# Kernel optimization log

Hardware: AMD Instinct MI355X
Metric: run time of the kernel (lower is better)

Reference implementation:

```python
import jax, jax.numpy as jnp
import numpy as np

KG_E = 50000
KG_R = 500
E_DIM = 300
NE = 400000      # entity-entity adjacency nnz
NEER = 400000    # entity-entity-relation triples
ALPHA1 = 0.1
ALPHA2 = 0.3
LRELU_ALPHA = 0.2


def setup_inputs() -> dict:
    key = jax.random.key(0)
    ks = jax.random.split(key, 13)
    primal_e_0 = jax.random.normal(ks[0], (KG_E, E_DIM), jnp.float32)
    # sparse-ish relation->entity incidence matrices (dense storage as in torch code)
    r_head = (jax.random.uniform(ks[1], (KG_R, KG_E)) < 0.01).astype(jnp.float32)
    r_tail = (jax.random.uniform(ks[2], (KG_R, KG_E)) < 0.01).astype(jnp.float32)
    e_adj_index = jax.random.randint(ks[3], (2, NE), 0, KG_E)
    e_adj_data = jax.random.uniform(ks[4], (NE,), jnp.float32)
    eer_adj_index = jax.random.randint(ks[5], (2, NEER), 0, KG_E)
    eer_adj_data = jax.random.randint(ks[6], (NEER,), 0, KG_R)
    s = 0.05
    be_L = jax.random.normal(ks[7], (KG_E, 1), jnp.float32) * s
    be_R = jax.random.normal(ks[8], (KG_E, 1), jnp.float32) * s
    atten_r = jax.random.normal(ks[9], (2 * E_DIM, 1), jnp.float32) * s
    gcnW1 = jax.random.normal(ks[10], (E_DIM, E_DIM), jnp.float32) * s
    highwayWr = jax.random.normal(ks[11], (E_DIM, E_DIM), jnp.float32) * s
    highwaybr = jax.random.normal(ks[12], (E_DIM, 1), jnp.float32) * s
    return {"primal_e_0": primal_e_0, "r_head": r_head, "r_tail": r_tail,
            "e_adj_data": e_adj_data, "be_L": be_L, "be_R": be_R,
            "atten_r": atten_r, "gcnW1": gcnW1, "highwayWr": highwayWr,
            "highwaybr": highwaybr, "e_adj_index": e_adj_index,
            "eer_adj_index": eer_adj_index, "eer_adj_data": eer_adj_data}


def _spmm(idx, data, x):
    # sparse [KG_E, KG_E] (COO rows=idx[0], cols=idx[1], vals=data) @ dense x
    rows, cols = idx[0], idx[1]
    return jax.ops.segment_sum(data[:, None] * x[cols], rows, num_segments=KG_E)


def _inv_or_zero(x):
    return jnp.where(x == 0, 0.0, 1.0 / x)


def _add_r_layer(e, be_L, be_R, r_head, r_tail, rh_inv, rt_inv):
    L_r = (r_head @ (e * be_L)) * rh_inv   # [KG_R, E_DIM]
    R_r = (r_tail @ (e * be_R)) * rt_inv
    return jax.nn.relu(jnp.concatenate([L_r, R_r], axis=-1))  # [KG_R, 2*E_DIM]


def _add_e_att_layer(e, r_layer, eer_idx, eer_rel, atten_r):
    rows, cols = eer_idx[0], eer_idx[1]
    e_ij = jnp.concatenate([e[rows], e[cols]], axis=1)           # [NEER, 2*E_DIM]
    eer_embed = e_ij * r_layer[eer_rel]                           # [NEER, 2*E_DIM]
    score = (eer_embed @ atten_r)[:, 0]                           # [NEER]
    ee_atten = jnp.exp(-jax.nn.leaky_relu(score, LRELU_ALPHA))
    e_rowsum = jax.ops.segment_sum(ee_atten, rows, num_segments=KG_E)[:, None]
    e_rowsum = _inv_or_zero(e_rowsum)
    e_out = jax.ops.segment_sum(ee_atten[:, None] * e[cols], rows, num_segments=KG_E)
    return jax.nn.relu(e_out * e_rowsum)


def _add_diag_layer(e, gcnW1, e_adj_index, e_adj_data):
    # dropout p=0 (eval) -> identity
    return jax.nn.relu(_spmm(e_adj_index, e_adj_data, e @ gcnW1))


def _highway(e1, e2, Wr, br):
    gate = jax.nn.sigmoid(e1 @ Wr + br[:, 0])
    return gate * e2 + (1.0 - gate) * e1


def reference(primal_e_0, r_head, r_tail, e_adj_data, be_L, be_R, atten_r,
              gcnW1, highwayWr, highwaybr, e_adj_index, eer_adj_index,
              eer_adj_data):
    rh_inv = _inv_or_zero(jnp.sum(r_head, axis=-1, keepdims=True))
    rt_inv = _inv_or_zero(jnp.sum(r_tail, axis=-1, keepdims=True))
    name_embed = primal_e_0
    r1 = _add_r_layer(name_embed, be_L, be_R, r_head, r_tail, rh_inv, rt_inv)
    e1 = _add_e_att_layer(name_embed, r1, eer_adj_index, eer_adj_data, atten_r)
    e1 = name_embed + ALPHA1 * e1
    r2 = _add_r_layer(e1, be_L, be_R, r_head, r_tail, rh_inv, rt_inv)
    e2 = _add_e_att_layer(e1, r2, eer_adj_index, eer_adj_data, atten_r)
    e2 = name_embed + ALPHA2 * e2
    g1 = _add_diag_layer(e2, gcnW1, e_adj_index, e_adj_data)
    g2 = _highway(e2, g1, highwayWr, highwaybr)
    g3 = _add_diag_layer(g2, gcnW1, e_adj_index, e_adj_data)
    return _highway(g2, g3, highwayWr, highwaybr)
```

## Files before the change

### kernel.cpp

```cpp
#include <hip/hip_runtime.h>
#include <math.h>

#define KG_E  50000
#define KG_R  500
#define E_DIM 300
#define NPAIR 150
#define NP2   75
#define CAP   1024
#define LRELU 0.2f

#define NK    10
#define NT    40
#define XS_LD 328

#define NB_SCAN 49

typedef __attribute__((ext_vector_type(8))) short bf16x8;
typedef __attribute__((ext_vector_type(4))) float f32x4;

__device__ __forceinline__ unsigned short f2bf(float x) {
  union { float f; unsigned u; } v; v.f = x;
  unsigned r = v.u + 0x7FFFu + ((v.u >> 16) & 1u);
  return (unsigned short)(r >> 16);
}
__device__ __forceinline__ float bf2f(unsigned short x) {
  union { unsigned u; float f; } v; v.u = ((unsigned)x) << 16; return v.f;
}
__device__ __forceinline__ float plo(unsigned u) {
  union { unsigned u; float f; } v; v.u = u << 16; return v.f;
}
__device__ __forceinline__ float phi(unsigned u) {
  union { unsigned u; float f; } v; v.u = u & 0xFFFF0000u; return v.f;
}
__device__ __forceinline__ unsigned packbf(float lo, float hi) {
  return (unsigned)f2bf(lo) | ((unsigned)f2bf(hi) << 16);
}

__global__ __launch_bounds__(256) void k_tobf(
    const float* __restrict__ src, unsigned short* __restrict__ dst, int n4)
{
  int i = blockIdx.x * 256 + threadIdx.x;
  if (i >= n4) return;
  float4 f = ((const float4*)src)[i];
  ushort4 o;
  o.x = f2bf(f.x); o.y = f2bf(f.y); o.z = f2bf(f.z); o.w = f2bf(f.w);
  ((ushort4*)dst)[i] = o;
}

#define NCH 5
#define SCAP 1024
__global__ __launch_bounds__(256) void k_compact2(
    const float* __restrict__ r_head, const float* __restrict__ r_tail,
    const float* __restrict__ be_L, const float* __restrict__ be_R,
    int* __restrict__ lidx, float* __restrict__ lsval,
    int* __restrict__ fill, float* __restrict__ rsum)
{
  __shared__ int   ls_e[SCAP];
  __shared__ float ls_v[SCAP];
  __shared__ int   ls_cnt;
  __shared__ float ls_sum;
  __shared__ int   ls_base;
  int m = blockIdx.z;
  int r = blockIdx.y;
  const float* rowp = (m ? r_tail : r_head) + (size_t)r * KG_E;
  const float* be   = m ? be_R : be_L;
  int slot = m * KG_R + r;
  int lane = threadIdx.x & 63;
  if (threadIdx.x == 0) { ls_cnt = 0; ls_sum = 0.f; }
  __syncthreads();

  const int CH = KG_E / NCH;
  int c0 = blockIdx.x * CH;
  const float4* rp4 = (const float4*)(rowp + c0);
  float lsum = 0.f;
  for (int i = threadIdx.x; i < CH / 4; i += 256) {
    float4 f = rp4[i];
    float vs[4] = {f.x, f.y, f.z, f.w};
    #pragma unroll
    for (int q = 0; q < 4; ++q) {
      float v = vs[q];
      lsum += v;
      bool nz = (v != 0.f);
      unsigned long long mask = __ballot(nz);
      if (mask) {
        int leader = (int)__ffsll(mask) - 1;
        int wbase = 0;
        if (lane == leader) wbase = atomicAdd(&ls_cnt, (int)__popcll(mask));
        wbase = __shfl(wbase, leader, 64);
        if (nz) {
          int pos = wbase + (int)__popcll(mask & ((1ULL << lane) - 1));
          if (pos < SCAP) {
            int e = c0 + 4 * i + q;
            ls_e[pos] = e;
            ls_v[pos] = v * be[e];
          }
        }
      }
    }
  }
  #pragma unroll
  for (int off = 32; off > 0; off >>= 1) lsum += __shfl_xor(lsum, off, 64);
  if (lane == 0 && lsum != 0.f) atomicAdd(&ls_sum, lsum);
  __syncthreads();

  int total = ls_cnt < SCAP ? ls_cnt : SCAP;
  if (threadIdx.x == 0) {
    ls_base = atomicAdd(&fill[slot], total);
    if (ls_sum != 0.f) atomicAdd(&rsum[slot], ls_sum);
  }
  __syncthreads();
  int gbase = ls_base;
  int*   li = lidx  + (size_t)slot * CAP;
  float* lv = lsval + (size_t)slot * CAP;
  for (int i = threadIdx.x; i < total; i += 256) {
    int pos = gbase + i;
    if (pos < CAP) { li[pos] = ls_e[i]; lv[pos] = ls_v[i]; }
  }
}

__global__ __launch_bounds__(256) void k_rmeta(
    const int* __restrict__ fill, const float* __restrict__ rsum,
    int* __restrict__ cnt, float* __restrict__ inv)
{
  int i = blockIdx.x * 256 + threadIdx.x;
  if (i < 2 * KG_R) {
    int c = fill[i];
    cnt[i] = c > CAP ? CAP : c;
    float s = rsum[i];
    inv[i] = (s == 0.f) ? 0.f : 1.f / s;
  }
}

__global__ __launch_bounds__(192) void k_rlayer(
    const unsigned short* __restrict__ Eb, const int* __restrict__ lidx,
    const float* __restrict__ lsval, const int* __restrict__ cnt,
    const float* __restrict__ inv, const float* __restrict__ atten,
    unsigned* __restrict__ wpk)
{
  int b = blockIdx.x;
  int m = b / KG_R, r = b % KG_R;
  int p = threadIdx.x;
  if (p >= NPAIR) return;
  int slot = m * KG_R + r;
  int n = cnt[slot];
  const int*   li = lidx  + (size_t)slot * CAP;
  const float* lv = lsval + (size_t)slot * CAP;
  float alo = 0.f, ahi = 0.f;
  #pragma unroll 4
  for (int i = 0; i < n; ++i) {
    int e = li[i];
    float s = lv[i];
    unsigned u = ((const unsigned*)(Eb + (size_t)e * E_DIM))[p];
    alo += s * plo(u);
    ahi += s * phi(u);
  }
  float iv = inv[slot];
  float vlo = alo * iv; vlo = vlo > 0.f ? vlo : 0.f;
  float vhi = ahi * iv; vhi = vhi > 0.f ? vhi : 0.f;
  vlo *= atten[m * E_DIM + 2 * p];
  vhi *= atten[m * E_DIM + 2 * p + 1];
  wpk[(size_t)slot * NPAIR + p] = packbf(vlo, vhi);
}

__global__ __launch_bounds__(256) void k_hist(
    const int* __restrict__ rows, int* __restrict__ cnt, int n)
{
  int i = blockIdx.x * 256 + threadIdx.x;
  if (i < n) atomicAdd(&cnt[rows[i]], 1);
}

__global__ __launch_bounds__(256) void k_scan_a(
    const int* __restrict__ c0, const int* __restrict__ c1,
    int* __restrict__ bsum, int n)
{
  const int* c = blockIdx.y ? c1 : c0;
  int base = blockIdx.x * 1024;
  int s = 0;
  #pragma unroll
  for (int k = 0; k < 4; ++k) {
    int i = base + k * 256 + threadIdx.x;
    if (i < n) s += c[i];
  }
  #pragma unroll
  for (int off = 32; off > 0; off >>= 1) s += __shfl_xor(s, off, 64);
  __shared__ int ws[4];
  if ((threadIdx.x & 63) == 0) ws[threadIdx.x >> 6] = s;
  __syncthreads();
  if (threadIdx.x == 0)
    bsum[blockIdx.y * (NB_SCAN + 1) + blockIdx.x] = ws[0] + ws[1] + ws[2] + ws[3];
}

__global__ __launch_bounds__(64) void k_scan_b(int* __restrict__ bsum)
{
  if (threadIdx.x < 2) {
    int* b = bsum + threadIdx.x * (NB_SCAN + 1);
    int acc = 0;
    for (int i = 0; i < NB_SCAN; ++i) { int v = b[i]; b[i] = acc; acc += v; }
    b[NB_SCAN] = acc;
  }
}

__global__ __launch_bounds__(256) void k_scan_c(
    const int* __restrict__ c0, const int* __restrict__ c1,
    const int* __restrict__ bsum,
    int* __restrict__ s0, int* __restrict__ s1, int n)
{
  const int* c = blockIdx.y ? c1 : c0;
  int* sO = blockIdx.y ? s1 : s0;
  if (blockIdx.x == 0 && threadIdx.x == 0)
    sO[n] = bsum[blockIdx.y * (NB_SCAN + 1) + NB_SCAN];
  int boff = bsum[blockIdx.y * (NB_SCAN + 1) + blockIdx.x];
  int i0 = blockIdx.x * 1024 + threadIdx.x * 4;
  int4 v = {0, 0, 0, 0};
  if (i0 < n) v = ((const int4*)c)[i0 >> 2];
  int tsum = v.x + v.y + v.z + v.w;
  int lane = threadIdx.x & 63, wid = threadIdx.x >> 6;
  int inc = tsum;
  #pragma unroll
  for (int off = 1; off < 64; off <<= 1) {
    int u = __shfl_up(inc, off, 64);
    if (lane >= off) inc += u;
  }
  __shared__ int ws[4];
  if (lane == 63) ws[wid] = inc;
  __syncthreads();
  int woff = 0;
  if (wid > 0) woff += ws[0];
  if (wid > 1) woff += ws[1];
  if (wid > 2) woff += ws[2];
  int ex = boff + woff + inc - tsum;
  if (i0 < n) {
    int4 o;
    o.x = ex; o.y = ex + v.x; o.z = o.y + v.y; o.w = o.z + v.z;
    ((int4*)sO)[i0 >> 2] = o;
  }
}

__global__ __launch_bounds__(256) void k_scatter_eer(
    const int* __restrict__ eidx, const int* __restrict__ erel,
    const int* __restrict__ start, int* __restrict__ fill,
    int* __restrict__ scol, int* __restrict__ srel, int neer)
{
  int i = blockIdx.x * 256 + threadIdx.x;
  if (i >= neer) return;
  int row = eidx[i];
  int pos = start[row] + atomicAdd(&fill[row], 1);
  scol[pos] = eidx[neer + i];
  srel[pos] = erel[i];
}

__global__ __launch_bounds__(256) void k_scatter_adj(
    const int* __restrict__ aidx, const float* __restrict__ adata,
    const int* __restrict__ start, int* __restrict__ fill,
    int* __restrict__ scol, float* __restrict__ sval, int ne)
{
  int i = blockIdx.x * 256 + threadIdx.x;
  if (i >= ne) return;
  int row = aidx[i];
  int pos = start[row] + atomicAdd(&fill[row], 1);
  scol[pos] = aidx[ne + i];
  sval[pos] = adata[i];
}

__global__ __launch_bounds__(256) void k_att_csr(
    const unsigned short* __restrict__ Eb, const unsigned* __restrict__ wpk,
    const int* __restrict__ start, const int* __restrict__ scol,
    const int* __restrict__ srel, const unsigned short* __restrict__ baseb,
    float alpha, unsigned short* __restrict__ outb)
{
  int wave = threadIdx.x >> 6, lane = threadIdx.x & 63;
  int half = lane >> 5, hl = lane & 31;
  int row = blockIdx.x * 4 + wave;
  if (row >= KG_E) return;
  int s = start[row], e = start[row + 1];
  const uint2* erp = (const uint2*)(Eb + (size_t)row * E_DIM);
  float er0[3], er1[3], er2[3], er3[3];
  float ac0[3] = {0,0,0}, ac1[3] = {0,0,0}, ac2[3] = {0,0,0}, ac3[3] = {0,0,0};
  #pragma unroll
  for (int c = 0; c < 3; ++c) {
    int m = c * 32 + hl;
    if (m < NP2) {
      uint2 u = erp[m];
      er0[c] = plo(u.x); er1[c] = phi(u.x); er2[c] = plo(u.y); er3[c] = phi(u.y);
    } else { er0[c] = er1[c] = er2[c] = er3[c] = 0.f; }
  }
  float rs = 0.f;
  int nIter = (e - s + 1) >> 1;
  for (int it = 0; it < nIter; ++it) {
    int j = s + 2 * it + half;
    bool act = j < e;
    int col = act ? scol[j] : 0;
    int rel = act ? srel[j] : 0;
    const uint2* ecp = (const uint2*)(Eb + (size_t)col * E_DIM);
    const uint2* whp = (const uint2*)(wpk + (size_t)rel * NPAIR);
    const uint2* wtp = (const uint2*)(wpk + (size_t)(KG_R + rel) * NPAIR);
    float e0[3], e1[3], e2[3], e3[3];
    float p4 = 0.f;
    #pragma unroll
    for (int c = 0; c < 3; ++c) {
      int m = c * 32 + hl;
      if (m < NP2) {
        uint2 uc = ecp[m], uh = whp[m], ut = wtp[m];
        float c0 = plo(uc.x), c1 = phi(uc.x), c2 = plo(uc.y), c3 = phi(uc.y);
        e0[c] = c0; e1[c] = c1; e2[c] = c2; e3[c] = c3;
        p4 += er0[c] * plo(uh.x) + er1[c] * phi(uh.x)
            + er2[c] * plo(uh.y) + er3[c] * phi(uh.y)
            + c0 * plo(ut.x) + c1 * phi(ut.x)
            + c2 * plo(ut.y) + c3 * phi(ut.y);
      } else { e0[c] = e1[c] = e2[c] = e3[c] = 0.f; }
    }
    #pragma unroll
    for (int off = 16; off > 0; off >>= 1) p4 += __shfl_xor(p4, off, 64);
    float la = p4 >= 0.f ? p4 : LRELU * p4;
    float at = act ? __expf(-la) : 0.f;
    rs += at;
    #pragma unroll
    for (int c = 0; c < 3; ++c) {
      ac0[c] += at * e0[c]; ac1[c] += at * e1[c];
      ac2[c] += at * e2[c]; ac3[c] += at * e3[c];
    }
  }
  rs += __shfl_xor(rs, 32, 64);
  #pragma unroll
  for (int c = 0; c < 3; ++c) {
    ac0[c] += __shfl_xor(ac0[c], 32, 64);
    ac1[c] += __shfl_xor(ac1[c], 32, 64);
    ac2[c] += __shfl_xor(ac2[c], 32, 64);
    ac3[c] += __shfl_xor(ac3[c], 32, 64);
  }
  if (half == 0) {
    float iv = (rs == 0.f) ? 0.f : 1.f / rs;
    const uint2* bp = (const uint2*)(baseb + (size_t)row * E_DIM);
    uint2* op = (uint2*)(outb + (size_t)row * E_DIM);
    #pragma unroll
    for (int c = 0; c < 3; ++c) {
      int m = c * 32 + hl;
      if (m < NP2) {
        uint2 ub = bp[m];
        float v0 = ac0[c] * iv; v0 = v0 > 0.f ? v0 : 0.f;
        float v1 = ac1[c] * iv; v1 = v1 > 0.f ? v1 : 0.f;
        float v2 = ac2[c] * iv; v2 = v2 > 0.f ? v2 : 0.f;
        float v3 = ac3[c] * iv; v3 = v3 > 0.f ? v3 : 0.f;
        uint2 o2;
        o2.x = packbf(plo(ub.x) + alpha * v0, phi(ub.x) + alpha * v1);
        o2.y = packbf(plo(ub.y) + alpha * v2, phi(ub.y) + alpha * v3);
        op[m] = o2;
      }
    }
  }
}

__global__ __launch_bounds__(256) void k_spmm_hw(
    const unsigned short* __restrict__ Xb, const int* __restrict__ start,
    const int* __restrict__ scol, const float* __restrict__ sval,
    const unsigned short* __restrict__ Gb, const unsigned short* __restrict__ baseb,
    const float* __restrict__ br,
    unsigned short* __restrict__ outb, float* __restrict__ outf)
{
  int wave = threadIdx.x >> 6, lane = threadIdx.x & 63;
  int half = lane >> 5, hl = lane & 31;
  int row = blockIdx.x * 4 + wave;
  if (row >= KG_E) return;
  int s = start[row], e = start[row + 1];
  float ac0[3] = {0,0,0}, ac1[3] = {0,0,0}, ac2[3] = {0,0,0}, ac3[3] = {0,0,0};
  int nIter = (e - s + 1) >> 1;
  for (int it = 0; it < nIter; ++it) {
    int j = s + 2 * it + half;
    bool act = j < e;
    int col = act ? scol[j] : 0;
    float v = act ? sval[j] : 0.f;
    const uint2* xp = (const uint2*)(Xb + (size_t)col * E_DIM);
    #pragma unroll
    for (int c = 0; c < 3; ++c) {
      int m = c * 32 + hl;
      if (m < NP2) {
        uint2 u = xp[m];
        ac0[c] += v * plo(u.x); ac1[c] += v * phi(u.x);
        ac2[c] += v * plo(u.y); ac3[c] += v * phi(u.y);
      }
    }
  }
  #pragma unroll
  for (int c = 0; c < 3; ++c) {
    ac0[c] += __shfl_xor(ac0[c], 32, 64);
    ac1[c] += __shfl_xor(ac1[c], 32, 64);
    ac2[c] += __shfl_xor(ac2[c], 32, 64);
    ac3[c] += __shfl_xor(ac3[c], 32, 64);
  }
  if (half == 0) {
    const uint2* gp = (const uint2*)(Gb + (size_t)row * E_DIM);
    const uint2* bp = (const uint2*)(baseb + (size_t)row * E_DIM);
    #pragma unroll
    for (int c = 0; c < 3; ++c) {
      int m = c * 32 + hl;
      if (m < NP2) {
        uint2 ug = gp[m], ub = bp[m];
        float4 b4 = ((const float4*)br)[m];
        float g0 = 1.f / (1.f + __expf(-(plo(ug.x) + b4.x)));
        float g1 = 1.f / (1.f + __expf(-(phi(ug.x) + b4.y)));
        float g2 = 1.f / (1.f + __expf(-(plo(ug.y) + b4.z)));
        float g3 = 1.f / (1.f + __expf(-(phi(ug.y) + b4.w)));
        float y0 = ac0[c] > 0.f ? ac0[c] : 0.f;
        float y1 = ac1[c] > 0.f ? ac1[c] : 0.f;
        float y2 = ac2[c] > 0.f ? ac2[c] : 0.f;
        float y3 = ac3[c] > 0.f ? ac3[c] : 0.f;
        float o0 = g0 * y0 + (1.f - g0) * plo(ub.x);
        float o1 = g1 * y1 + (1.f - g1) * phi(ub.x);
        float o2 = g2 * y2 + (1.f - g2) * plo(ub.y);
        float o3 = g3 * y3 + (1.f - g3) * phi(ub.y);
        if (outb) {
          uint2 ov;
          ov.x = packbf(o0, o1); ov.y = packbf(o2, o3);
          ((uint2*)(outb + (size_t)row * E_DIM))[m] = ov;
        } else {
          float4 of; of.x = o0; of.y = o1; of.z = o2; of.w = o3;
          ((float4*)(outf + (size_t)row * E_DIM))[m] = of;
        }
      }
    }
  }
}

__global__ __launch_bounds__(64) void k_packW(
    const float* __restrict__ W1, const float* __restrict__ W2,
    unsigned short* __restrict__ Wp)
{
  int lane = threadIdx.x;
  int t = blockIdx.x, s = blockIdx.y;
  int c = t * 16 + (lane & 15);
  unsigned short v[8];
  #pragma unroll
  for (int j = 0; j < 8; ++j) {
    int k = s * 32 + (lane >> 4) * 8 + j;
    float x = 0.f;
    if (k < E_DIM && c < 2 * E_DIM)
      x = (c < E_DIM) ? W1[(size_t)k * E_DIM + c]
                      : W2[(size_t)k * E_DIM + (c - E_DIM)];
    v[j] = f2bf(x);
  }
  size_t base = ((size_t)(t * NK + s) * 64 + lane) * 8;
  #pragma unroll
  for (int j = 0; j < 8; ++j) Wp[base + j] = v[j];
}

__global__ __launch_bounds__(256) void k_gemm2_mfma(
    const unsigned short* __restrict__ Xb, const unsigned short* __restrict__ Wp,
    unsigned short* __restrict__ Y1, unsigned short* __restrict__ Y2, int M)
{
  __shared__ unsigned short Xs[32][XS_LD];
  int tid = threadIdx.x;
  int r0 = blockIdx.x * 32;
  int nb = blockIdx.y;

  for (int t = tid; t < 32 * (XS_LD / 2); t += 256) {
    int r = t / (XS_LD / 2), u = t % (XS_LD / 2);
    unsigned v = 0;
    int rg = r0 + r;
    if (rg < M && u < E_DIM / 2) v = ((const unsigned*)Xb)[(size_t)rg * (E_DIM / 2) + u];
    ((unsigned*)&Xs[0][0])[r * (XS_LD / 2) + u] = v;
  }
  __syncthreads();

  int wid = tid >> 6, lane = tid & 63;
  int wave_m = wid >> 1, wave_n = wid & 1;
  int rowA = wave_m * 16 + (lane & 15);
  int kgrp = (lane >> 4) * 8;
  int tb0 = nb * 8 + wave_n * 4;

  const bf16x8* wfrag = (const bf16x8*)Wp + (size_t)tb0 * (NK * 64) + lane;

  f32x4 acc[4] = {{0,0,0,0},{0,0,0,0},{0,0,0,0},{0,0,0,0}};
  #pragma unroll 2
  for (int ks = 0; ks < NK; ++ks) {
    bf16x8 a = *(const bf16x8*)&Xs[rowA][ks * 32 + kgrp];
    #pragma unroll
    for (int nt = 0; nt < 4; ++nt) {
      bf16x8 b = wfrag[(nt * NK + ks) * 64];
      acc[nt] = __builtin_amdgcn_mfma_f32_16x16x32_bf16(a, b, acc[nt], 0, 0, 0);
    }
  }

  int rbase = r0 + wave_m * 16 + ((lane >> 4) << 2);
  #pragma unroll
  for (int nt = 0; nt < 4; ++nt) {
    int c = (tb0 + nt) * 16 + (lane & 15);
    #pragma unroll
    for (int j = 0; j < 4; ++j) {
      int row = rbase + j;
      if (row < M) {
        unsigned short hv = f2bf(acc[nt][j]);
        if (c < E_DIM)            Y1[(size_t)row * E_DIM + c] = hv;
        else if (c < 2 * E_DIM)   Y2[(size_t)row * E_DIM + (c - E_DIM)] = hv;
      }
    }
  }
}

extern "C" void kernel_launch(void* const* d_in, const int* in_sizes, int n_in,
                              void* d_out, int out_size, void* d_ws, size_t ws_size,
                              hipStream_t stream)
{
  const float* primal      = (const float*)d_in[0];
  const float* r_head      = (const float*)d_in[1];
  const float* r_tail      = (const float*)d_in[2];
  const float* e_adj_data  = (const float*)d_in[3];
  const float* be_L        = (const float*)d_in[4];
  const float* be_R        = (const float*)d_in[5];
  const float* atten_r     = (const float*)d_in[6];
  const float* gcnW1       = (const float*)d_in[7];
  const float* hwWr        = (const float*)d_in[8];
  const float* hwbr        = (const float*)d_in[9];
  const int*   e_adj_index = (const int*)d_in[10];
  const int*   eer_idx     = (const int*)d_in[11];
  const int*   eer_rel     = (const int*)d_in[12];
  int ne   = in_sizes[10] / 2;
  int neer = in_sizes[11] / 2;

  char* ws = (char*)d_ws;
  size_t off = 0;
  auto take = [&](size_t bytes) {
    void* p = ws + off;
    off = (off + bytes + 255) & ~(size_t)255;
    return p;
  };
  int*   cnt      = (int*)  take((size_t)2 * KG_R * sizeof(int));
  float* inv      = (float*)take((size_t)2 * KG_R * sizeof(float));
  size_t z0 = off;
  int*   hcntA    = (int*)  take((size_t)KG_E * sizeof(int));
  int*   hcntB    = (int*)  take((size_t)KG_E * sizeof(int));
  int*   hfillA   = (int*)  take((size_t)KG_E * sizeof(int));
  int*   hfillB   = (int*)  take((size_t)KG_E * sizeof(int));
  int*   rfill    = (int*)  take((size_t)2 * KG_R * sizeof(int));
  float* rsumb    = (float*)take((size_t)2 * KG_R * sizeof(float));
  size_t z1 = off;
  int*   lidx     = (int*)  take((size_t)2 * KG_R * CAP * sizeof(int));
  float* lsv      = (float*)take((size_t)2 * KG_R * CAP * sizeof(float));
  unsigned* wpk   = (unsigned*)take((size_t)2 * KG_R * NPAIR * sizeof(unsigned));
  int*   bsum     = (int*)  take((size_t)2 * (NB_SCAN + 1) * sizeof(int));
  int*   eer_start= (int*)  take((size_t)(KG_E + 4) * sizeof(int));
  int*   adj_start= (int*)  take((size_t)(KG_E + 4) * sizeof(int));
  int*   eer_scol = (int*)  take((size_t)neer * sizeof(int));
  int*   eer_srel = (int*)  take((size_t)neer * sizeof(int));
  int*   adj_scol = (int*)  take((size_t)ne * sizeof(int));
  float* adj_sval = (float*)take((size_t)ne * sizeof(float));
  unsigned short* Wp = (unsigned short*)take((size_t)NT * NK * 64 * 8 * sizeof(unsigned short));
  unsigned short* B0 = (unsigned short*)take((size_t)KG_E * E_DIM * sizeof(unsigned short));
  unsigned short* B1 = (unsigned short*)take((size_t)KG_E * E_DIM * sizeof(unsigned short));
  unsigned short* B2 = (unsigned short*)take((size_t)KG_E * E_DIM * sizeof(unsigned short));
  unsigned short* Fb = (unsigned short*)take((size_t)KG_E * E_DIM * sizeof(unsigned short));
  unsigned short* Gb = (unsigned short*)take((size_t)KG_E * E_DIM * sizeof(unsigned short));
  float* out      = (float*)d_out;
  (void)ws_size; (void)n_in; (void)out_size;

  int eg = (neer + 255) / 256;
  int ag = (ne + 255) / 256;

  hipMemsetAsync(ws + z0, 0, z1 - z0, stream);

  k_hist<<<eg, 256, 0, stream>>>(eer_idx, hcntA, neer);
  k_hist<<<ag, 256, 0, stream>>>(e_adj_index, hcntB, ne);
  k_scan_a<<<dim3(NB_SCAN, 2), 256, 0, stream>>>(hcntA, hcntB, bsum, KG_E);
  k_scan_b<<<1, 64, 0, stream>>>(bsum);
  k_scan_c<<<dim3(NB_SCAN, 2), 256, 0, stream>>>(hcntA, hcntB, bsum,
                                                 eer_start, adj_start, KG_E);
  k_scatter_eer<<<eg, 256, 0, stream>>>(eer_idx, eer_rel, eer_start, hfillA,
                                        eer_scol, eer_srel, neer);
  k_scatter_adj<<<ag, 256, 0, stream>>>(e_adj_index, e_adj_data, adj_start, hfillB,
                                        adj_scol, adj_sval, ne);

  k_compact2<<<dim3(NCH, KG_R, 2), 256, 0, stream>>>(r_head, r_tail, be_L, be_R,
                                                     lidx, lsv, rfill, rsumb);
  k_rmeta<<<(2 * KG_R + 255) / 256, 256, 0, stream>>>(rfill, rsumb, cnt, inv);
  k_packW<<<dim3(NT, NK), 64, 0, stream>>>(gcnW1, hwWr, Wp);
  int n4 = KG_E * E_DIM / 4;
  k_tobf<<<(n4 + 255) / 256, 256, 0, stream>>>(primal, B0, n4);

  int rg = (KG_E + 3) / 4;

  k_rlayer<<<2 * KG_R, 192, 0, stream>>>(B0, lidx, lsv, cnt, inv, atten_r, wpk);
  k_att_csr<<<rg, 256, 0, stream>>>(B0, wpk, eer_start, eer_scol, eer_srel,
                                    B0, 0.1f, B1);
  k_rlayer<<<2 * KG_R, 192, 0, stream>>>(B1, lidx, lsv, cnt, inv, atten_r, wpk);
  k_att_csr<<<rg, 256, 0, stream>>>(B1, wpk, eer_start, eer_scol, eer_srel,
                                    B0, 0.3f, B2);

  dim3 gg((KG_E + 31) / 32, 5);
  k_gemm2_mfma<<<gg, 256, 0, stream>>>(B2, Wp, Fb, Gb, KG_E);
  k_spmm_hw<<<rg, 256, 0, stream>>>(Fb, adj_start, adj_scol, adj_sval,
                                    Gb, B2, hwbr, B1, (float*)nullptr);

  k_gemm2_mfma<<<gg, 256, 0, stream>>>(B1, Wp, Fb, Gb, KG_E);
  k_spmm_hw<<<rg, 256, 0, stream>>>(Fb, adj_start, adj_scol, adj_sval,
                                    Gb, B1, hwbr, (unsigned short*)nullptr, out);
}
```

Measured before the change: 830.9 us.

## Switch intermediate storage and attention math from bf16 to fp16 packed ops

Changes every bf16 intermediate buffer, the packed weights and the MFMA GEMM to fp16, and does the attention kernel's dot products and weighted accumulation with packed half2 FMAs instead of scalar fp32. The aim is to cut per-edge ALU work in the gather-heavy attention kernel and to use cheaper packed conversions. It adds risk of precision loss or overflow, since attention accumulators now sum in fp16, and fp16 has a narrower range than bf16.

```diff
diff --git a/kernel.cpp b/kernel.cpp
--- a/kernel.cpp
+++ b/kernel.cpp
@@ -1,4 +1,5 @@
 #include <hip/hip_runtime.h>
+#include <hip/hip_fp16.h>
 #include <math.h>
 
 #define KG_E  50000
@@ -15,36 +16,31 @@
 
 #define NB_SCAN 49
 
-typedef __attribute__((ext_vector_type(8))) short bf16x8;
+typedef __attribute__((ext_vector_type(8))) _Float16 f16x8;
 typedef __attribute__((ext_vector_type(4))) float f32x4;
 
-__device__ __forceinline__ unsigned short f2bf(float x) {
-  union { float f; unsigned u; } v; v.f = x;
-  unsigned r = v.u + 0x7FFFu + ((v.u >> 16) & 1u);
-  return (unsigned short)(r >> 16);
-}
-__device__ __forceinline__ float bf2f(unsigned short x) {
-  union { unsigned u; float f; } v; v.u = ((unsigned)x) << 16; return v.f;
-}
-__device__ __forceinline__ float plo(unsigned u) {
-  union { unsigned u; float f; } v; v.u = u << 16; return v.f;
-}
-__device__ __forceinline__ float phi(unsigned u) {
-  union { unsigned u; float f; } v; v.u = u & 0xFFFF0000u; return v.f;
-}
-__device__ __forceinline__ unsigned packbf(float lo, float hi) {
-  return (unsigned)f2bf(lo) | ((unsigned)f2bf(hi) << 16);
-}
-
-__global__ __launch_bounds__(256) void k_tobf(
-    const float* __restrict__ src, unsigned short* __restrict__ dst, int n4)
+__device__ __forceinline__ __half2 u2h2(unsigned u) {
+  union { unsigned u; __half2 h; } v; v.u = u; return v.h;
+}
+__device__ __forceinline__ unsigned h22u(__half2 h) {
+  union { unsigned u; __half2 h; } v; v.h = h; return v.u;
+}
+__device__ __forceinline__ float hlo(unsigned u) { return __low2float(u2h2(u)); }
+__device__ __forceinline__ float hhi(unsigned u) { return __high2float(u2h2(u)); }
+__device__ __forceinline__ unsigned packh(float lo, float hi) {
+  return h22u(__floats2half2_rn(lo, hi));
+}
+
+__global__ __launch_bounds__(256) void k_toh(
+    const float* __restrict__ src, __half* __restrict__ dst, int n4)
 {
   int i = blockIdx.x * 256 + threadIdx.x;
   if (i >= n4) return;
   float4 f = ((const float4*)src)[i];
-  ushort4 o;
-  o.x = f2bf(f.x); o.y = f2bf(f.y); o.z = f2bf(f.z); o.w = f2bf(f.w);
-  ((ushort4*)dst)[i] = o;
+  uint2 o;
+  o.x = packh(f.x, f.y);
+  o.y = packh(f.z, f.w);
+  ((uint2*)dst)[i] = o;
 }
 
 #define NCH 5
@@ -132,7 +128,7 @@
 }
 
 __global__ __launch_bounds__(192) void k_rlayer(
-    const unsigned short* __restrict__ Eb, const int* __restrict__ lidx,
+    const __half* __restrict__ Eb, const int* __restrict__ lidx,
     const float* __restrict__ lsval, const int* __restrict__ cnt,
     const float* __restrict__ inv, const float* __restrict__ atten,
     unsigned* __restrict__ wpk)
@@ -151,15 +147,15 @@
     int e = li[i];
     float s = lv[i];
     unsigned u = ((const unsigned*)(Eb + (size_t)e * E_DIM))[p];
-    alo += s * plo(u);
-    ahi += s * phi(u);
+    alo += s * hlo(u);
+    ahi += s * hhi(u);
   }
   float iv = inv[slot];
   float vlo = alo * iv; vlo = vlo > 0.f ? vlo : 0.f;
   float vhi = ahi * iv; vhi = vhi > 0.f ? vhi : 0.f;
   vlo *= atten[m * E_DIM + 2 * p];
   vhi *= atten[m * E_DIM + 2 * p + 1];
-  wpk[(size_t)slot * NPAIR + p] = packbf(vlo, vhi);
+  wpk[(size_t)slot * NPAIR + p] = packh(vlo, vhi);
 }
 
 __global__ __launch_bounds__(256) void k_hist(
@@ -263,10 +259,10 @@
 }
 
 __global__ __launch_bounds__(256) void k_att_csr(
-    const unsigned short* __restrict__ Eb, const unsigned* __restrict__ wpk,
+    const __half* __restrict__ Eb, const unsigned* __restrict__ wpk,
     const int* __restrict__ start, const int* __restrict__ scol,
-    const int* __restrict__ srel, const unsigned short* __restrict__ baseb,
-    float alpha, unsigned short* __restrict__ outb)
+    const int* __restrict__ srel, const __half* __restrict__ baseb,
+    float alpha, __half* __restrict__ outb)
 {
   int wave = threadIdx.x >> 6, lane = threadIdx.x & 63;
   int half = lane >> 5, hl = lane & 31;
@@ -274,15 +270,16 @@
   if (row >= KG_E) return;
   int s = start[row], e = start[row + 1];
   const uint2* erp = (const uint2*)(Eb + (size_t)row * E_DIM);
-  float er0[3], er1[3], er2[3], er3[3];
-  float ac0[3] = {0,0,0}, ac1[3] = {0,0,0}, ac2[3] = {0,0,0}, ac3[3] = {0,0,0};
+  __half2 zero2 = __floats2half2_rn(0.f, 0.f);
+  __half2 er[3][2], ac[3][2];
   #pragma unroll
   for (int c = 0; c < 3; ++c) {
     int m = c * 32 + hl;
     if (m < NP2) {
       uint2 u = erp[m];
-      er0[c] = plo(u.x); er1[c] = phi(u.x); er2[c] = plo(u.y); er3[c] = phi(u.y);
-    } else { er0[c] = er1[c] = er2[c] = er3[c] = 0.f; }
+      er[c][0] = u2h2(u.x); er[c][1] = u2h2(u.y);
+    } else { er[c][0] = zero2; er[c][1] = zero2; }
+    ac[c][0] = zero2; ac[c][1] = zero2;
   }
   float rs = 0.f;
   int nIter = (e - s + 1) >> 1;
@@ -294,39 +291,41 @@
     const uint2* ecp = (const uint2*)(Eb + (size_t)col * E_DIM);
     const uint2* whp = (const uint2*)(wpk + (size_t)rel * NPAIR);
     const uint2* wtp = (const uint2*)(wpk + (size_t)(KG_R + rel) * NPAIR);
-    float e0[3], e1[3], e2[3], e3[3];
-    float p4 = 0.f;
+    __half2 ec[3][2];
+    __half2 p2 = zero2;
     #pragma unroll
     for (int c = 0; c < 3; ++c) {
       int m = c * 32 + hl;
       if (m < NP2) {
         uint2 uc = ecp[m], uh = whp[m], ut = wtp[m];
-        float c0 = plo(uc.x), c1 = phi(uc.x), c2 = plo(uc.y), c3 = phi(uc.y);
-        e0[c] = c0; e1[c] = c1; e2[c] = c2; e3[c] = c3;
-        p4 += er0[c] * plo(uh.x) + er1[c] * phi(uh.x)
-            + er2[c] * plo(uh.y) + er3[c] * phi(uh.y)
-            + c0 * plo(ut.x) + c1 * phi(ut.x)
-            + c2 * plo(ut.y) + c3 * phi(ut.y);
-      } else { e0[c] = e1[c] = e2[c] = e3[c] = 0.f; }
-    }
+        ec[c][0] = u2h2(uc.x); ec[c][1] = u2h2(uc.y);
+        p2 = __hfma2(er[c][0], u2h2(uh.x), p2);
+        p2 = __hfma2(er[c][1], u2h2(uh.y), p2);
+        p2 = __hfma2(ec[c][0], u2h2(ut.x), p2);
+        p2 = __hfma2(ec[c][1], u2h2(ut.y), p2);
+      } else { ec[c][0] = zero2; ec[c][1] = zero2; }
+    }
+    float p4 = __low2float(p2) + __high2float(p2);
     #pragma unroll
     for (int off = 16; off > 0; off >>= 1) p4 += __shfl_xor(p4, off, 64);
     float la = p4 >= 0.f ? p4 : LRELU * p4;
     float at = act ? __expf(-la) : 0.f;
     rs += at;
+    __half2 at2 = __float2half2_rn(at);
     #pragma unroll
     for (int c = 0; c < 3; ++c) {
-      ac0[c] += at * e0[c]; ac1[c] += at * e1[c];
-      ac2[c] += at * e2[c]; ac3[c] += at * e3[c];
+      ac[c][0] = __hfma2(at2, ec[c][0], ac[c][0]);
+      ac[c][1] = __hfma2(at2, ec[c][1], ac[c][1]);
     }
   }
   rs += __shfl_xor(rs, 32, 64);
   #pragma unroll
   for (int c = 0; c < 3; ++c) {
-    ac0[c] += __shfl_xor(ac0[c], 32, 64);
-    ac1[c] += __shfl_xor(ac1[c], 32, 64);
-    ac2[c] += __shfl_xor(ac2[c], 32, 64);
-    ac3[c] += __shfl_xor(ac3[c], 32, 64);
+    #pragma unroll
+    for (int k = 0; k < 2; ++k) {
+      unsigned o = __shfl_xor(h22u(ac[c][k]), 32, 64);
+      ac[c][k] = __hadd2(ac[c][k], u2h2(o));
+    }
   }
   if (half == 0) {
     float iv = (rs == 0.f) ? 0.f : 1.f / rs;
@@ -337,13 +336,13 @@
       int m = c * 32 + hl;
       if (m < NP2) {
         uint2 ub = bp[m];
-        float v0 = ac0[c] * iv; v0 = v0 > 0.f ? v0 : 0.f;
-        float v1 = ac1[c] * iv; v1 = v1 > 0.f ? v1 : 0.f;
-        float v2 = ac2[c] * iv; v2 = v2 > 0.f ? v2 : 0.f;
-        float v3 = ac3[c] * iv; v3 = v3 > 0.f ? v3 : 0.f;
+        float v0 = __low2float(ac[c][0]) * iv;  v0 = v0 > 0.f ? v0 : 0.f;
+        float v1 = __high2float(ac[c][0]) * iv; v1 = v1 > 0.f ? v1 : 0.f;
+        float v2 = __low2float(ac[c][1]) * iv;  v2 = v2 > 0.f ? v2 : 0.f;
+        float v3 = __high2float(ac[c][1]) * iv; v3 = v3 > 0.f ? v3 : 0.f;
         uint2 o2;
-        o2.x = packbf(plo(ub.x) + alpha * v0, phi(ub.x) + alpha * v1);
-        o2.y = packbf(plo(ub.y) + alpha * v2, phi(ub.y) + alpha * v3);
+        o2.x = packh(hlo(ub.x) + alpha * v0, hhi(ub.x) + alpha * v1);
+        o2.y = packh(hlo(ub.y) + alpha * v2, hhi(ub.y) + alpha * v3);
         op[m] = o2;
       }
     }
@@ -351,11 +350,11 @@
 }
 
 __global__ __launch_bounds__(256) void k_spmm_hw(
-    const unsigned short* __restrict__ Xb, const int* __restrict__ start,
+    const __half* __restrict__ Xb, const int* __restrict__ start,
     const int* __restrict__ scol, const float* __restrict__ sval,
-    const unsigned short* __restrict__ Gb, const unsigned short* __restrict__ baseb,
+    const __half* __restrict__ Gb, const __half* __restrict__ baseb,
     const float* __restrict__ br,
-    unsigned short* __restrict__ outb, float* __restrict__ outf)
+    __half* __restrict__ outb, float* __restrict__ outf)
 {
   int wave = threadIdx.x >> 6, lane = threadIdx.x & 63;
   int half = lane >> 5, hl = lane & 31;
@@ -375,8 +374,8 @@
       int m = c * 32 + hl;
       if (m < NP2) {
         uint2 u = xp[m];
-        ac0[c] += v * plo(u.x); ac1[c] += v * phi(u.x);
-        ac2[c] += v * plo(u.y); ac3[c] += v * phi(u.y);
+        ac0[c] += v * hlo(u.x); ac1[c] += v * hhi(u.x);
+        ac2[c] += v * hlo(u.y); ac3[c] += v * hhi(u.y);
       }
     }
   }
@@ -396,21 +395,21 @@
       if (m < NP2) {
         uint2 ug = gp[m], ub = bp[m];
         float4 b4 = ((const float4*)br)[m];
-        float g0 = 1.f / (1.f + __expf(-(plo(ug.x) + b4.x)));
-        float g1 = 1.f / (1.f + __expf(-(phi(ug.x) + b4.y)));
-        float g2 = 1.f / (1.f + __expf(-(plo(ug.y) + b4.z)));
-        float g3 = 1.f / (1.f + __expf(-(phi(ug.y) + b4.w)));
+        float g0 = 1.f / (1.f + __expf(-(hlo(ug.x) + b4.x)));
+        float g1 = 1.f / (1.f + __expf(-(hhi(ug.x) + b4.y)));
+        float g2 = 1.f / (1.f + __expf(-(hlo(ug.y) + b4.z)));
+        float g3 = 1.f / (1.f + __expf(-(hhi(ug.y) + b4.w)));
         float y0 = ac0[c] > 0.f ? ac0[c] : 0.f;
         float y1 = ac1[c] > 0.f ? ac1[c] : 0.f;
         float y2 = ac2[c] > 0.f ? ac2[c] : 0.f;
         float y3 = ac3[c] > 0.f ? ac3[c] : 0.f;
-        float o0 = g0 * y0 + (1.f - g0) * plo(ub.x);
-        float o1 = g1 * y1 + (1.f - g1) * phi(ub.x);
-        float o2 = g2 * y2 + (1.f - g2) * plo(ub.y);
-        float o3 = g3 * y3 + (1.f - g3) * phi(ub.y);
+        float o0 = g0 * y0 + (1.f - g0) * hlo(ub.x);
+        float o1 = g1 * y1 + (1.f - g1) * hhi(ub.x);
+        float o2 = g2 * y2 + (1.f - g2) * hlo(ub.y);
+        float o3 = g3 * y3 + (1.f - g3) * hhi(ub.y);
         if (outb) {
           uint2 ov;
-          ov.x = packbf(o0, o1); ov.y = packbf(o2, o3);
+          ov.x = packh(o0, o1); ov.y = packh(o2, o3);
           ((uint2*)(outb + (size_t)row * E_DIM))[m] = ov;
         } else {
           float4 of; of.x = o0; of.y = o1; of.z = o2; of.w = o3;
@@ -423,12 +422,12 @@
 
 __global__ __launch_bounds__(64) void k_packW(
     const float* __restrict__ W1, const float* __restrict__ W2,
-    unsigned short* __restrict__ Wp)
+    __half* __restrict__ Wp)
 {
   int lane = threadIdx.x;
   int t = blockIdx.x, s = blockIdx.y;
   int c = t * 16 + (lane & 15);
-  unsigned short v[8];
+  __half v[8];
   #pragma unroll
   for (int j = 0; j < 8; ++j) {
     int k = s * 32 + (lane >> 4) * 8 + j;
@@ -436,7 +435,7 @@
     if (k < E_DIM && c < 2 * E_DIM)
       x = (c < E_DIM) ? W1[(size_t)k * E_DIM + c]
                       : W2[(size_t)k * E_DIM + (c - E_DIM)];
-    v[j] = f2bf(x);
+    v[j] = __float2half_rn(x);
   }
   size_t base = ((size_t)(t * NK + s) * 64 + lane) * 8;
   #pragma unroll
@@ -444,10 +443,10 @@
 }
 
 __global__ __launch_bounds__(256) void k_gemm2_mfma(
-    const unsigned short* __restrict__ Xb, const unsigned short* __restrict__ Wp,
-    unsigned short* __restrict__ Y1, unsigned short* __restrict__ Y2, int M)
-{
-  __shared__ unsigned short Xs[32][XS_LD];
+    const __half* __restrict__ Xb, const __half* __restrict__ Wp,
+    __half* __restrict__ Y1, __half* __restrict__ Y2, int M)
+{
+  __shared__ __half Xs[32][XS_LD];
   int tid = threadIdx.x;
   int r0 = blockIdx.x * 32;
   int nb = blockIdx.y;
@@ -467,16 +466,16 @@
   int kgrp = (lane >> 4) * 8;
   int tb0 = nb * 8 + wave_n * 4;
 
-  const bf16x8* wfrag = (const bf16x8*)Wp + (size_t)tb0 * (NK * 64) + lane;
+  const f16x8* wfrag = (const f16x8*)Wp + (size_t)tb0 * (NK * 64) + lane;
 
   f32x4 acc[4] = {{0,0,0,0},{0,0,0,0},{0,0,0,0},{0,0,0,0}};
   #pragma unroll 2
   for (int ks = 0; ks < NK; ++ks) {
-    bf16x8 a = *(const bf16x8*)&Xs[rowA][ks * 32 + kgrp];
+    f16x8 a = *(const f16x8*)&Xs[rowA][ks * 32 + kgrp];
     #pragma unroll
     for (int nt = 0; nt < 4; ++nt) {
-      bf16x8 b = wfrag[(nt * NK + ks) * 64];
-      acc[nt] = __builtin_amdgcn_mfma_f32_16x16x32_bf16(a, b, acc[nt], 0, 0, 0);
+      f16x8 b = wfrag[(nt * NK + ks) * 64];
+      acc[nt] = __builtin_amdgcn_mfma_f32_16x16x32_f16(a, b, acc[nt], 0, 0, 0);
     }
   }
 
@@ -488,7 +487,7 @@
     for (int j = 0; j < 4; ++j) {
       int row = rbase + j;
       if (row < M) {
-        unsigned short hv = f2bf(acc[nt][j]);
+        __half hv = __float2half_rn(acc[nt][j]);
         if (c < E_DIM)            Y1[(size_t)row * E_DIM + c] = hv;
         else if (c < 2 * E_DIM)   Y2[(size_t)row * E_DIM + (c - E_DIM)] = hv;
       }
@@ -543,12 +542,12 @@
   int*   eer_srel = (int*)  take((size_t)neer * sizeof(int));
   int*   adj_scol = (int*)  take((size_t)ne * sizeof(int));
   float* adj_sval = (float*)take((size_t)ne * sizeof(float));
-  unsigned short* Wp = (unsigned short*)take((size_t)NT * NK * 64 * 8 * sizeof(unsigned short));
-  unsigned short* B0 = (unsigned short*)take((size_t)KG_E * E_DIM * sizeof(unsigned short));
-  unsigned short* B1 = (unsigned short*)take((size_t)KG_E * E_DIM * sizeof(unsigned short));
-  unsigned short* B2 = (unsigned short*)take((size_t)KG_E * E_DIM * sizeof(unsigned short));
-  unsigned short* Fb = (unsigned short*)take((size_t)KG_E * E_DIM * sizeof(unsigned short));
-  unsigned short* Gb = (unsigned short*)take((size_t)KG_E * E_DIM * sizeof(unsigned short));
+  __half* Wp = (__half*)take((size_t)NT * NK * 64 * 8 * sizeof(__half));
+  __half* B0 = (__half*)take((size_t)KG_E * E_DIM * sizeof(__half));
+  __half* B1 = (__half*)take((size_t)KG_E * E_DIM * sizeof(__half));
+  __half* B2 = (__half*)take((size_t)KG_E * E_DIM * sizeof(__half));
+  __half* Fb = (__half*)take((size_t)KG_E * E_DIM * sizeof(__half));
+  __half* Gb = (__half*)take((size_t)KG_E * E_DIM * sizeof(__half));
   float* out      = (float*)d_out;
   (void)ws_size; (void)n_in; (void)out_size;
 
@@ -573,7 +572,7 @@
   k_rmeta<<<(2 * KG_R + 255) / 256, 256, 0, stream>>>(rfill, rsumb, cnt, inv);
   k_packW<<<dim3(NT, NK), 64, 0, stream>>>(gcnW1, hwWr, Wp);
   int n4 = KG_E * E_DIM / 4;
-  k_tobf<<<(n4 + 255) / 256, 256, 0, stream>>>(primal, B0, n4);
+  k_toh<<<(n4 + 255) / 256, 256, 0, stream>>>(primal, B0, n4);
 
   int rg = (KG_E + 3) / 4;
 
@@ -591,5 +590,5 @@
 
   k_gemm2_mfma<<<gg, 256, 0, stream>>>(B1, Wp, Fb, Gb, KG_E);
   k_spmm_hw<<<rg, 256, 0, stream>>>(Fb, adj_start, adj_scol, adj_sval,
-                                    Gb, B1, hwbr, (unsigned short*)nullptr, out);
-}
+                                    Gb, B1, hwbr, (__half*)nullptr, out);
+}
```

Measured after the change: 803.0 us. 1.03x faster.
